# Kernel tuning notes

Measured on AMD Instinct MI355X. Metric: run time of the kernel, lower is better.

The kernel has to match this reference:

```python
import jax, jax.numpy as jnp
import numpy as np

N_EDGES = 1_600_000
N_NODES = 100_000
N_GRAPH = 8
D_EDGE = 16
D_NODE = 16
D_GLOB = 16
D_IN = D_EDGE + 2 * D_NODE + D_GLOB  # 64, concat width
D_HID = 64
D_OUT = 16


def setup_inputs() -> dict:
    key = jax.random.key(0)
    ks = jax.random.split(key, 12)
    edges = jax.random.normal(ks[0], (N_EDGES, D_EDGE), dtype=jnp.float32)
    nodes = jax.random.normal(ks[1], (N_NODES, D_NODE), dtype=jnp.float32)
    globals_ = jax.random.normal(ks[2], (N_GRAPH, D_GLOB), dtype=jnp.float32)
    senders = jax.random.randint(ks[3], (N_EDGES,), 0, N_NODES, dtype=jnp.int32)
    receivers = jax.random.randint(ks[4], (N_EDGES,), 0, N_NODES, dtype=jnp.int32)
    edge_graph_ids = jnp.sort(jax.random.randint(ks[5], (N_EDGES,), 0, N_GRAPH, dtype=jnp.int32))
    s0 = 1.0 / np.sqrt(D_IN)
    s1 = 1.0 / np.sqrt(D_HID)
    W0 = jax.random.uniform(ks[6], (D_IN, D_HID), jnp.float32, -s0, s0)
    b0 = jax.random.uniform(ks[7], (D_HID,), jnp.float32, -s0, s0)
    W1 = jax.random.uniform(ks[8], (D_HID, D_HID), jnp.float32, -s1, s1)
    b1 = jax.random.uniform(ks[9], (D_HID,), jnp.float32, -s1, s1)
    W2 = jax.random.uniform(ks[10], (D_HID, D_OUT), jnp.float32, -s1, s1)
    b2 = jax.random.uniform(ks[11], (D_OUT,), jnp.float32, -s1, s1)
    return {"edges": edges, "nodes": nodes, "globals_": globals_,
            "W0": W0, "b0": b0, "W1": W1, "b1": b1, "W2": W2, "b2": b2,
            "senders": senders, "receivers": receivers,
            "edge_graph_ids": edge_graph_ids}


def reference(edges, nodes, globals_, W0, b0, W1, b1, W2, b2,
              senders, receivers, edge_graph_ids):
    # broadcast_receiver/sender_nodes_to_edges: gather node feats per edge
    recv = jnp.take(nodes, receivers, axis=0)          # [E, D_NODE]
    send = jnp.take(nodes, senders, axis=0)            # [E, D_NODE]
    # broadcast_globals_to_edges: repeat(globals, n_edge) == gather by graph id
    glob = jnp.take(globals_, edge_graph_ids, axis=0)  # [E, D_GLOB]
    x = jnp.concatenate([edges, recv, send, glob], axis=-1)  # [E, 64]
    # edge MLP: two hidden relu blocks then output linear (norm='none')
    h = jax.nn.relu(x @ W0 + b0)
    h = jax.nn.relu(h @ W1 + b1)
    return h @ W2 + b2  # updated edges [E, D_OUT]
```

## Files before the change

kernel.cpp:

```cpp
#include <hip/hip_runtime.h>


typedef float f32x4 __attribute__((ext_vector_type(4)));
typedef short short8 __attribute__((ext_vector_type(8)));

#define E_DIV16(x) ((x) >> 4)

__device__ __forceinline__ unsigned short f2bf(float f) {
    union { float f; unsigned int u; } v; v.f = f;
    unsigned int u = v.u;
    u += 0x7FFFu + ((u >> 16) & 1u);
    return (unsigned short)(u >> 16);
}
__device__ __forceinline__ float bf2f(unsigned short b) {
    union { unsigned int u; float f; } v; v.u = ((unsigned int)b) << 16;
    return v.f;
}

__global__ void prep_kernel(const float* __restrict__ W0, const float* __restrict__ b0,
                            const float* __restrict__ W1, const float* __restrict__ b1,
                            const float* __restrict__ W2, const float* __restrict__ b2,
                            void* __restrict__ ws) {
    unsigned short* w0h = (unsigned short*)ws;
    unsigned short* w0l = w0h + 4096;
    unsigned short* w1h = w0h + 8192;
    unsigned short* w1l = w0h + 12288;
    unsigned short* w2h = w0h + 16384;
    unsigned short* w2l = w0h + 17408;
    float* b0f = (float*)(w0h + 18432);
    float* b1f = b0f + 1024;
    float* b2f = b0f + 2048;
    const int tid = threadIdx.x;

    for (int idx = tid; idx < 4096; idx += 256) {
        int j = idx & 7, lane = (idx >> 3) & 63, f = idx >> 9;
        int t = f >> 1, kt = f & 1, mr = lane & 15, g = lane >> 4;
        float w = W0[(32 * kt + 8 * g + j) * 64 + (16 * t + mr)];
        unsigned short h = f2bf(w);
        w0h[idx] = h;
        w0l[idx] = f2bf(w - bf2f(h));
    }
    for (int idx = tid; idx < 4096; idx += 256) {
        int j = idx & 7, lane = (idx >> 3) & 63, f = idx >> 9;
        int t = f >> 1, kt = f & 1, mr = lane & 15, g = lane >> 4;
        int mu = 16 * (2 * kt + (j >> 2)) + 4 * g + (j & 3);
        float w = W1[mu * 64 + (16 * t + mr)];
        unsigned short h = f2bf(w);
        w1h[idx] = h;
        w1l[idx] = f2bf(w - bf2f(h));
    }
    for (int idx = tid; idx < 1024; idx += 256) {
        int j = idx & 7, lane = (idx >> 3) & 63, kt = idx >> 9;
        int mr = lane & 15, g = lane >> 4;
        int mu = 16 * (2 * kt + (j >> 2)) + 4 * g + (j & 3);
        float w = W2[mu * 16 + mr];
        unsigned short h = f2bf(w);
        w2h[idx] = h;
        w2l[idx] = f2bf(w - bf2f(h));
    }
    for (int idx = tid; idx < 1024; idx += 256) {
        int lane = idx >> 4, tr = idx & 15;
        int g = lane >> 4, t = tr >> 2, r = tr & 3;
        b0f[idx] = b0[16 * t + 4 * g + r];
        b1f[idx] = b1[16 * t + 4 * g + r];
    }
    for (int idx = tid; idx < 256; idx += 256) {
        int lane = idx >> 2, r = idx & 3, g = lane >> 4;
        b2f[idx] = b2[4 * g + r];
    }
}

__global__ __launch_bounds__(256, 2) void edge_mlp_kernel(
    const float* __restrict__ edges, const float* __restrict__ nodes,
    const float* __restrict__ globals_, const int* __restrict__ senders,
    const int* __restrict__ receivers, const int* __restrict__ gids,
    const void* __restrict__ ws, float* __restrict__ out, int n_tiles) {

    const unsigned short* w0h = (const unsigned short*)ws;
    const unsigned short* w0l = w0h + 4096;
    const unsigned short* w1h = w0h + 8192;
    const unsigned short* w1l = w0h + 12288;
    const unsigned short* w2h = w0h + 16384;
    const unsigned short* w2l = w0h + 17408;
    const float* b0f = (const float*)(w0h + 18432);
    const float* b1f = b0f + 1024;
    const float* b2f = b0f + 2048;

    const int lane = threadIdx.x & 63;
    const int wv = threadIdx.x >> 6;
    const int mr = lane & 15;
    const int g = lane >> 4;

    short8 W0H[4][2], W0L[4][2], W1H[4][2], W1L[4][2], W2H[2], W2L[2];
#pragma unroll
    for (int t = 0; t < 4; ++t)
#pragma unroll
        for (int kt = 0; kt < 2; ++kt) {
            int o = ((t * 2 + kt) * 64 + lane) * 8;
            W0H[t][kt] = *(const short8*)(w0h + o);
            W0L[t][kt] = *(const short8*)(w0l + o);
            W1H[t][kt] = *(const short8*)(w1h + o);
            W1L[t][kt] = *(const short8*)(w1l + o);
        }
#pragma unroll
    for (int kt = 0; kt < 2; ++kt) {
        int o = (kt * 64 + lane) * 8;
        W2H[kt] = *(const short8*)(w2h + o);
        W2L[kt] = *(const short8*)(w2l + o);
    }
    float B0[16], B1[16], B2[4];
#pragma unroll
    for (int i = 0; i < 16; ++i) { B0[i] = b0f[lane * 16 + i]; B1[i] = b1f[lane * 16 + i]; }
#pragma unroll
    for (int i = 0; i < 4; ++i) B2[i] = b2f[lane * 4 + i];

    const int stride = gridDim.x * 4;
    for (int tile = blockIdx.x * 4 + wv; tile < n_tiles; tile += stride) {
        const int e = tile * 16 + mr;
        const int ri = receivers[e];
        const int si = senders[e];
        const int gi = gids[e];

        const float* p0 = (g < 2) ? (edges + (size_t)e * 16 + 8 * g)
                                  : (nodes + (size_t)ri * 16 + 8 * (g - 2));
        const float* p1 = (g < 2) ? (nodes + (size_t)si * 16 + 8 * g)
                                  : (globals_ + (size_t)gi * 16 + 8 * (g - 2));
        f32x4 x0 = *(const f32x4*)p0;
        f32x4 x1 = *(const f32x4*)(p0 + 4);
        f32x4 x2 = *(const f32x4*)p1;
        f32x4 x3 = *(const f32x4*)(p1 + 4);

        float xs[16];
#pragma unroll
        for (int i = 0; i < 4; ++i) { xs[i] = x0[i]; xs[4 + i] = x1[i]; xs[8 + i] = x2[i]; xs[12 + i] = x3[i]; }
        short8 XH[2], XL[2];
#pragma unroll
        for (int kt = 0; kt < 2; ++kt)
#pragma unroll
            for (int j = 0; j < 8; ++j) {
                float v = xs[kt * 8 + j];
                unsigned short h = f2bf(v);
                XH[kt][j] = (short)h;
                XL[kt][j] = (short)f2bf(v - bf2f(h));
            }

        f32x4 acc0[4];
#pragma unroll
        for (int t = 0; t < 4; ++t) {
            f32x4 a = {0.f, 0.f, 0.f, 0.f};
            a = __builtin_amdgcn_mfma_f32_16x16x32_bf16(W0L[t][0], XH[0], a, 0, 0, 0);
            a = __builtin_amdgcn_mfma_f32_16x16x32_bf16(W0L[t][1], XH[1], a, 0, 0, 0);
            a = __builtin_amdgcn_mfma_f32_16x16x32_bf16(W0H[t][0], XL[0], a, 0, 0, 0);
            a = __builtin_amdgcn_mfma_f32_16x16x32_bf16(W0H[t][1], XL[1], a, 0, 0, 0);
            a = __builtin_amdgcn_mfma_f32_16x16x32_bf16(W0H[t][0], XH[0], a, 0, 0, 0);
            a = __builtin_amdgcn_mfma_f32_16x16x32_bf16(W0H[t][1], XH[1], a, 0, 0, 0);
            acc0[t] = a;
        }

        short8 HH[2], HL[2];
#pragma unroll
        for (int t = 0; t < 4; ++t)
#pragma unroll
            for (int r = 0; r < 4; ++r) {
                float v = acc0[t][r] + B0[t * 4 + r];
                v = fmaxf(v, 0.0f);
                int kt = t >> 1;
                int j = ((t & 1) << 2) | r;
                unsigned short h = f2bf(v);
                HH[kt][j] = (short)h;
                HL[kt][j] = (short)f2bf(v - bf2f(h));
            }

        f32x4 acc1[4];
#pragma unroll
        for (int t = 0; t < 4; ++t) {
            f32x4 a = {0.f, 0.f, 0.f, 0.f};
            a = __builtin_amdgcn_mfma_f32_16x16x32_bf16(W1L[t][0], HH[0], a, 0, 0, 0);
            a = __builtin_amdgcn_mfma_f32_16x16x32_bf16(W1L[t][1], HH[1], a, 0, 0, 0);
            a = __builtin_amdgcn_mfma_f32_16x16x32_bf16(W1H[t][0], HL[0], a, 0, 0, 0);
            a = __builtin_amdgcn_mfma_f32_16x16x32_bf16(W1H[t][1], HL[1], a, 0, 0, 0);
            a = __builtin_amdgcn_mfma_f32_16x16x32_bf16(W1H[t][0], HH[0], a, 0, 0, 0);
            a = __builtin_amdgcn_mfma_f32_16x16x32_bf16(W1H[t][1], HH[1], a, 0, 0, 0);
            acc1[t] = a;
        }

        short8 GH[2], GL[2];
#pragma unroll
        for (int t = 0; t < 4; ++t)
#pragma unroll
            for (int r = 0; r < 4; ++r) {
                float v = acc1[t][r] + B1[t * 4 + r];
                v = fmaxf(v, 0.0f);
                int kt = t >> 1;
                int j = ((t & 1) << 2) | r;
                unsigned short h = f2bf(v);
                GH[kt][j] = (short)h;
                GL[kt][j] = (short)f2bf(v - bf2f(h));
            }

        f32x4 o = {0.f, 0.f, 0.f, 0.f};
        o = __builtin_amdgcn_mfma_f32_16x16x32_bf16(W2L[0], GH[0], o, 0, 0, 0);
        o = __builtin_amdgcn_mfma_f32_16x16x32_bf16(W2L[1], GH[1], o, 0, 0, 0);
        o = __builtin_amdgcn_mfma_f32_16x16x32_bf16(W2H[0], GL[0], o, 0, 0, 0);
        o = __builtin_amdgcn_mfma_f32_16x16x32_bf16(W2H[1], GL[1], o, 0, 0, 0);
        o = __builtin_amdgcn_mfma_f32_16x16x32_bf16(W2H[0], GH[0], o, 0, 0, 0);
        o = __builtin_amdgcn_mfma_f32_16x16x32_bf16(W2H[1], GH[1], o, 0, 0, 0);

        f32x4 res;
#pragma unroll
        for (int r = 0; r < 4; ++r) res[r] = o[r] + B2[r];
        *(f32x4*)(out + (size_t)e * 16 + 4 * g) = res;
    }
}

extern "C" void kernel_launch(void* const* d_in, const int* in_sizes, int n_in,
                              void* d_out, int out_size, void* d_ws, size_t ws_size,
                              hipStream_t stream) {
    const float* edges    = (const float*)d_in[0];
    const float* nodes    = (const float*)d_in[1];
    const float* globals_ = (const float*)d_in[2];
    const float* W0 = (const float*)d_in[3];
    const float* b0 = (const float*)d_in[4];
    const float* W1 = (const float*)d_in[5];
    const float* b1 = (const float*)d_in[6];
    const float* W2 = (const float*)d_in[7];
    const float* b2 = (const float*)d_in[8];
    const int* senders   = (const int*)d_in[9];
    const int* receivers = (const int*)d_in[10];
    const int* gids      = (const int*)d_in[11];
    float* out = (float*)d_out;

    const int n_edges = in_sizes[9];
    const int n_tiles = E_DIV16(n_edges);

    prep_kernel<<<1, 256, 0, stream>>>(W0, b0, W1, b1, W2, b2, d_ws);

    int grid = (n_tiles + 3) / 4;
    if (grid > 2048) grid = 2048;
    edge_mlp_kernel<<<grid, 256, 0, stream>>>(edges, nodes, globals_, senders, receivers,
                                              gids, d_ws, out, n_tiles);
}
```

Measured before the change: 325.9 us.

## Software-pipeline gathers across tiles, fold biases into MFMA accumulators, widen prep grid

Restructures the edge loop into a fixed-iteration software pipeline. The next tile's gathered features and the index loads two tiles ahead are issued before the current tile's MFMA chain, so gather latency overlaps with compute. Biases now seed the MFMA accumulators, the bf16 split uses HIP intrinsics, and outputs go out as nontemporal stores. The prep kernel runs on 72 blocks and the main grid becomes 2500 blocks. Out-of-range iterations are clamped to the last tile and recompute and rewrite it, and the extra live registers may lower occupancy.

```diff
diff --git a/kernel.cpp b/kernel.cpp
--- a/kernel.cpp
+++ b/kernel.cpp
@@ -1,10 +1,9 @@
 #include <hip/hip_runtime.h>
+#include <hip/hip_bf16.h>
 
 
 typedef float f32x4 __attribute__((ext_vector_type(4)));
 typedef short short8 __attribute__((ext_vector_type(8)));
-
-#define E_DIV16(x) ((x) >> 4)
 
 __device__ __forceinline__ unsigned short f2bf(float f) {
     union { float f; unsigned int u; } v; v.f = f;
@@ -15,6 +14,13 @@
 __device__ __forceinline__ float bf2f(unsigned short b) {
     union { unsigned int u; float f; } v; v.u = ((unsigned int)b) << 16;
     return v.f;
+}
+__device__ __forceinline__ void bfsplit(float v, unsigned short& h, unsigned short& l) {
+    union { __hip_bfloat16 b; unsigned short u; } ch, cl;
+    ch.b = __float2bfloat16(v);
+    float r = v - __bfloat162float(ch.b);
+    cl.b = __float2bfloat16(r);
+    h = ch.u; l = cl.u;
 }
 
 __global__ void prep_kernel(const float* __restrict__ W0, const float* __restrict__ b0,
@@ -30,9 +36,10 @@
     float* b0f = (float*)(w0h + 18432);
     float* b1f = b0f + 1024;
     float* b2f = b0f + 2048;
-    const int tid = threadIdx.x;
-
-    for (int idx = tid; idx < 4096; idx += 256) {
+    const int tid = blockIdx.x * blockDim.x + threadIdx.x;
+    const int gstride = gridDim.x * blockDim.x;
+
+    for (int idx = tid; idx < 4096; idx += gstride) {
         int j = idx & 7, lane = (idx >> 3) & 63, f = idx >> 9;
         int t = f >> 1, kt = f & 1, mr = lane & 15, g = lane >> 4;
         float w = W0[(32 * kt + 8 * g + j) * 64 + (16 * t + mr)];
@@ -40,7 +47,7 @@
         w0h[idx] = h;
         w0l[idx] = f2bf(w - bf2f(h));
     }
-    for (int idx = tid; idx < 4096; idx += 256) {
+    for (int idx = tid; idx < 4096; idx += gstride) {
         int j = idx & 7, lane = (idx >> 3) & 63, f = idx >> 9;
         int t = f >> 1, kt = f & 1, mr = lane & 15, g = lane >> 4;
         int mu = 16 * (2 * kt + (j >> 2)) + 4 * g + (j & 3);
@@ -49,7 +56,7 @@
         w1h[idx] = h;
         w1l[idx] = f2bf(w - bf2f(h));
     }
-    for (int idx = tid; idx < 1024; idx += 256) {
+    for (int idx = tid; idx < 1024; idx += gstride) {
         int j = idx & 7, lane = (idx >> 3) & 63, kt = idx >> 9;
         int mr = lane & 15, g = lane >> 4;
         int mu = 16 * (2 * kt + (j >> 2)) + 4 * g + (j & 3);
@@ -58,13 +65,13 @@
         w2h[idx] = h;
         w2l[idx] = f2bf(w - bf2f(h));
     }
-    for (int idx = tid; idx < 1024; idx += 256) {
+    for (int idx = tid; idx < 1024; idx += gstride) {
         int lane = idx >> 4, tr = idx & 15;
         int g = lane >> 4, t = tr >> 2, r = tr & 3;
         b0f[idx] = b0[16 * t + 4 * g + r];
         b1f[idx] = b1[16 * t + 4 * g + r];
     }
-    for (int idx = tid; idx < 256; idx += 256) {
+    for (int idx = tid; idx < 256; idx += gstride) {
         int lane = idx >> 2, r = idx & 3, g = lane >> 4;
         b2f[idx] = b2[4 * g + r];
     }
@@ -74,7 +81,7 @@
     const float* __restrict__ edges, const float* __restrict__ nodes,
     const float* __restrict__ globals_, const int* __restrict__ senders,
     const int* __restrict__ receivers, const int* __restrict__ gids,
-    const void* __restrict__ ws, float* __restrict__ out, int n_tiles) {
+    const void* __restrict__ ws, float* __restrict__ out, int n_tiles, int iters) {
 
     const unsigned short* w0h = (const unsigned short*)ws;
     const unsigned short* w0l = w0h + 4096;
@@ -114,91 +121,100 @@
 #pragma unroll
     for (int i = 0; i < 4; ++i) B2[i] = b2f[lane * 4 + i];
 
-    const int stride = gridDim.x * 4;
-    for (int tile = blockIdx.x * 4 + wv; tile < n_tiles; tile += stride) {
-        const int e = tile * 16 + mr;
-        const int ri = receivers[e];
-        const int si = senders[e];
-        const int gi = gids[e];
-
-        const float* p0 = (g < 2) ? (edges + (size_t)e * 16 + 8 * g)
-                                  : (nodes + (size_t)ri * 16 + 8 * (g - 2));
-        const float* p1 = (g < 2) ? (nodes + (size_t)si * 16 + 8 * g)
-                                  : (globals_ + (size_t)gi * 16 + 8 * (g - 2));
-        f32x4 x0 = *(const f32x4*)p0;
-        f32x4 x1 = *(const f32x4*)(p0 + 4);
-        f32x4 x2 = *(const f32x4*)p1;
-        f32x4 x3 = *(const f32x4*)(p1 + 4);
+    const int W = gridDim.x << 2;
+    const int wave_id = (blockIdx.x << 2) | wv;
+    const int last = n_tiles - 1;
+
+    #define TILE_OF(i) (((wave_id + (i) * W) < n_tiles) ? (wave_id + (i) * W) : last)
+
+    int e_cur = TILE_OF(0) * 16 + mr;
+    {
+        int ri = receivers[e_cur], si = senders[e_cur], gi = gids[e_cur];
+        (void)ri; (void)si; (void)gi;
+    }
+    int ri0 = receivers[e_cur], si0 = senders[e_cur], gi0 = gids[e_cur];
+    const float* p0 = (g < 2) ? (edges + (size_t)e_cur * 16 + 8 * g)
+                              : (nodes + (size_t)ri0 * 16 + 8 * (g - 2));
+    const float* p1 = (g < 2) ? (nodes + (size_t)si0 * 16 + 8 * g)
+                              : (globals_ + (size_t)gi0 * 16 + 8 * (g - 2));
+    f32x4 x0 = *(const f32x4*)p0;
+    f32x4 x1 = *(const f32x4*)(p0 + 4);
+    f32x4 x2 = *(const f32x4*)p1;
+    f32x4 x3 = *(const f32x4*)(p1 + 4);
+
+    int e_nxt = TILE_OF(1) * 16 + mr;
+    int ri_n = receivers[e_nxt], si_n = senders[e_nxt], gi_n = gids[e_nxt];
+
+    for (int i = 0; i < iters; ++i) {
+        const float* q0 = (g < 2) ? (edges + (size_t)e_nxt * 16 + 8 * g)
+                                  : (nodes + (size_t)ri_n * 16 + 8 * (g - 2));
+        const float* q1 = (g < 2) ? (nodes + (size_t)si_n * 16 + 8 * g)
+                                  : (globals_ + (size_t)gi_n * 16 + 8 * (g - 2));
+        f32x4 n0 = *(const f32x4*)q0;
+        f32x4 n1 = *(const f32x4*)(q0 + 4);
+        f32x4 n2 = *(const f32x4*)q1;
+        f32x4 n3 = *(const f32x4*)(q1 + 4);
+
+        int e_nn = TILE_OF(i + 2) * 16 + mr;
+        int ri_nn = receivers[e_nn], si_nn = senders[e_nn], gi_nn = gids[e_nn];
 
         float xs[16];
 #pragma unroll
-        for (int i = 0; i < 4; ++i) { xs[i] = x0[i]; xs[4 + i] = x1[i]; xs[8 + i] = x2[i]; xs[12 + i] = x3[i]; }
+        for (int k = 0; k < 4; ++k) { xs[k] = x0[k]; xs[4 + k] = x1[k]; xs[8 + k] = x2[k]; xs[12 + k] = x3[k]; }
         short8 XH[2], XL[2];
 #pragma unroll
         for (int kt = 0; kt < 2; ++kt)
 #pragma unroll
             for (int j = 0; j < 8; ++j) {
-                float v = xs[kt * 8 + j];
-                unsigned short h = f2bf(v);
+                unsigned short h, l;
+                bfsplit(xs[kt * 8 + j], h, l);
                 XH[kt][j] = (short)h;
-                XL[kt][j] = (short)f2bf(v - bf2f(h));
+                XL[kt][j] = (short)l;
             }
 
-        f32x4 acc0[4];
+        short8 HH[2], HL[2];
 #pragma unroll
         for (int t = 0; t < 4; ++t) {
-            f32x4 a = {0.f, 0.f, 0.f, 0.f};
+            f32x4 a = {B0[t * 4 + 0], B0[t * 4 + 1], B0[t * 4 + 2], B0[t * 4 + 3]};
             a = __builtin_amdgcn_mfma_f32_16x16x32_bf16(W0L[t][0], XH[0], a, 0, 0, 0);
             a = __builtin_amdgcn_mfma_f32_16x16x32_bf16(W0L[t][1], XH[1], a, 0, 0, 0);
             a = __builtin_amdgcn_mfma_f32_16x16x32_bf16(W0H[t][0], XL[0], a, 0, 0, 0);
             a = __builtin_amdgcn_mfma_f32_16x16x32_bf16(W0H[t][1], XL[1], a, 0, 0, 0);
             a = __builtin_amdgcn_mfma_f32_16x16x32_bf16(W0H[t][0], XH[0], a, 0, 0, 0);
             a = __builtin_amdgcn_mfma_f32_16x16x32_bf16(W0H[t][1], XH[1], a, 0, 0, 0);
-            acc0[t] = a;
+#pragma unroll
+            for (int r = 0; r < 4; ++r) {
+                float v = fmaxf(a[r], 0.0f);
+                int kt = t >> 1, j = ((t & 1) << 2) | r;
+                unsigned short h, l;
+                bfsplit(v, h, l);
+                HH[kt][j] = (short)h;
+                HL[kt][j] = (short)l;
+            }
         }
 
-        short8 HH[2], HL[2];
-#pragma unroll
-        for (int t = 0; t < 4; ++t)
-#pragma unroll
-            for (int r = 0; r < 4; ++r) {
-                float v = acc0[t][r] + B0[t * 4 + r];
-                v = fmaxf(v, 0.0f);
-                int kt = t >> 1;
-                int j = ((t & 1) << 2) | r;
-                unsigned short h = f2bf(v);
-                HH[kt][j] = (short)h;
-                HL[kt][j] = (short)f2bf(v - bf2f(h));
-            }
-
-        f32x4 acc1[4];
+        short8 GH[2], GL[2];
 #pragma unroll
         for (int t = 0; t < 4; ++t) {
-            f32x4 a = {0.f, 0.f, 0.f, 0.f};
+            f32x4 a = {B1[t * 4 + 0], B1[t * 4 + 1], B1[t * 4 + 2], B1[t * 4 + 3]};
             a = __builtin_amdgcn_mfma_f32_16x16x32_bf16(W1L[t][0], HH[0], a, 0, 0, 0);
             a = __builtin_amdgcn_mfma_f32_16x16x32_bf16(W1L[t][1], HH[1], a, 0, 0, 0);
             a = __builtin_amdgcn_mfma_f32_16x16x32_bf16(W1H[t][0], HL[0], a, 0, 0, 0);
             a = __builtin_amdgcn_mfma_f32_16x16x32_bf16(W1H[t][1], HL[1], a, 0, 0, 0);
             a = __builtin_amdgcn_mfma_f32_16x16x32_bf16(W1H[t][0], HH[0], a, 0, 0, 0);
             a = __builtin_amdgcn_mfma_f32_16x16x32_bf16(W1H[t][1], HH[1], a, 0, 0, 0);
-            acc1[t] = a;
+#pragma unroll
+            for (int r = 0; r < 4; ++r) {
+                float v = fmaxf(a[r], 0.0f);
+                int kt = t >> 1, j = ((t & 1) << 2) | r;
+                unsigned short h, l;
+                bfsplit(v, h, l);
+                GH[kt][j] = (short)h;
+                GL[kt][j] = (short)l;
+            }
         }
 
-        short8 GH[2], GL[2];
-#pragma unroll
-        for (int t = 0; t < 4; ++t)
-#pragma unroll
-            for (int r = 0; r < 4; ++r) {
-                float v = acc1[t][r] + B1[t * 4 + r];
-                v = fmaxf(v, 0.0f);
-                int kt = t >> 1;
-                int j = ((t & 1) << 2) | r;
-                unsigned short h = f2bf(v);
-                GH[kt][j] = (short)h;
-                GL[kt][j] = (short)f2bf(v - bf2f(h));
-            }
-
-        f32x4 o = {0.f, 0.f, 0.f, 0.f};
+        f32x4 o = {B2[0], B2[1], B2[2], B2[3]};
         o = __builtin_amdgcn_mfma_f32_16x16x32_bf16(W2L[0], GH[0], o, 0, 0, 0);
         o = __builtin_amdgcn_mfma_f32_16x16x32_bf16(W2L[1], GH[1], o, 0, 0, 0);
         o = __builtin_amdgcn_mfma_f32_16x16x32_bf16(W2H[0], GL[0], o, 0, 0, 0);
@@ -206,11 +222,13 @@
         o = __builtin_amdgcn_mfma_f32_16x16x32_bf16(W2H[0], GH[0], o, 0, 0, 0);
         o = __builtin_amdgcn_mfma_f32_16x16x32_bf16(W2H[1], GH[1], o, 0, 0, 0);
 
-        f32x4 res;
-#pragma unroll
-        for (int r = 0; r < 4; ++r) res[r] = o[r] + B2[r];
-        *(f32x4*)(out + (size_t)e * 16 + 4 * g) = res;
-    }
+        __builtin_nontemporal_store(o, (f32x4*)(out + (size_t)e_cur * 16 + 4 * g));
+
+        e_cur = e_nxt;
+        x0 = n0; x1 = n1; x2 = n2; x3 = n3;
+        e_nxt = e_nn; ri_n = ri_nn; si_n = si_nn; gi_n = gi_nn;
+    }
+    #undef TILE_OF
 }
 
 extern "C" void kernel_launch(void* const* d_in, const int* in_sizes, int n_in,
@@ -231,12 +249,14 @@
     float* out = (float*)d_out;
 
     const int n_edges = in_sizes[9];
-    const int n_tiles = E_DIV16(n_edges);
-
-    prep_kernel<<<1, 256, 0, stream>>>(W0, b0, W1, b1, W2, b2, d_ws);
-
-    int grid = (n_tiles + 3) / 4;
-    if (grid > 2048) grid = 2048;
+    const int n_tiles = n_edges >> 4;
+
+    prep_kernel<<<72, 256, 0, stream>>>(W0, b0, W1, b1, W2, b2, d_ws);
+
+    int grid = 2500;
+    if (grid > (n_tiles + 3) / 4) grid = (n_tiles + 3) / 4;
+    const int waves = grid * 4;
+    const int iters = (n_tiles + waves - 1) / waves;
     edge_mlp_kernel<<<grid, 256, 0, stream>>>(edges, nodes, globals_, senders, receivers,
-                                              gids, d_ws, out, n_tiles);
-}
+                                              gids, d_ws, out, n_tiles, iters);
+}
```

Measured after the change: 282.2 us. 13.4% less time.
